# Kernel optimization log

Hardware: AMD Instinct MI355X
Metric: run time of the kernel (lower is better)

## Reference

```python
import jax, jax.numpy as jnp
import numpy as np

N = 4096
K = 8


def setup_inputs() -> dict:
    key = jax.random.key(0)
    kA, kb, ka, kZ, kC = jax.random.split(key, 5)
    A = (jax.random.uniform(kA, (N, N)) < 0.01).astype(jnp.float32)
    beta = jax.random.normal(kb, (N,), dtype=jnp.float32)
    a = jax.random.normal(ka, (1,), dtype=jnp.float32)
    Z = jax.random.normal(kZ, (K, N), dtype=jnp.float32)
    C = jax.random.normal(kC, (N, K), dtype=jnp.float32)
    return {"A": A, "beta": beta, "a": a, "Z": Z, "C": C}


def reference(A, beta, a, Z, C):
    # beta_ij = beta_i + beta_j  -> [N, N]
    beta2 = beta[:, None] + beta[None, :]
    Zs = jax.nn.softmax(Z, axis=0)          # [K, N], softmax over archetypes
    Cs = jax.nn.softmax(C, axis=0)          # [N, K], softmax over nodes
    # M = (Zs @ Cs @ Zs).T -> [N, K] latent positions
    M = (Zs @ (Cs @ Zs)).T
    # Pairwise euclidean distance with the original's +1e-6 shift inside the square.
    diff = M[:, None, :] - M[None, :, :] + 1e-6   # [N, N, K]
    z_dist = jnp.sqrt(jnp.sum(diff * diff, axis=-1))  # [N, N]
    theta = beta2 - a[0] * z_dist
    sp = jax.nn.softplus(theta)
    # Zero the diagonal (theta - diag(diagonal(theta)) zeroes diag entries).
    d = jnp.arange(N)
    theta_off = theta.at[d, d].set(0.0)
    sp_off = sp.at[d, d].set(0.0)
    LL = jnp.sum(theta_off * A) - jnp.sum(sp_off)
    return LL
```

## Files before the change

kernel.cpp:

```cpp
#include <hip/hip_runtime.h>

#define N 4096
#define K 8
#define RB 64
#define CB 256
#define RCH 16
#define NCH (RB / RCH)
#define NPB 16

__device__ __forceinline__ float fast_exp2(float x) { return __builtin_amdgcn_exp2f(x); }
__device__ __forceinline__ float fast_log2(float x) { return __builtin_amdgcn_logf(x); }
__device__ __forceinline__ float fast_sqrt(float x) { return __builtin_amdgcn_sqrtf(x); }

__device__ __forceinline__ void load_lds_16B(const float* g, float* l) {
    __builtin_amdgcn_global_load_lds((const __attribute__((address_space(1))) void*)g,
                                     (__attribute__((address_space(3))) void*)l,
                                     16, 0, 0);
}

__global__ __launch_bounds__(256) void prep_stats(
    const float* __restrict__ Z, const float* __restrict__ C,
    float* __restrict__ ZsT, float* __restrict__ Upart, float* __restrict__ out)
{
    const int t = threadIdx.x;
    const int n = blockIdx.x * 256 + t;
    const float L2E = 1.44269504f;

    __shared__ float zsL[256 * K];
    __shared__ float eL[256 * K];
    __shared__ float red[4][64];

    if (blockIdx.x == 0 && t == 0) out[0] = 0.f;

    float z[K];
#pragma unroll
    for (int k = 0; k < K; ++k) z[k] = Z[k * N + n];
    float zmax = z[0];
#pragma unroll
    for (int k = 1; k < K; ++k) zmax = fmaxf(zmax, z[k]);
    float zs[K];
    float zsum = 0.f;
#pragma unroll
    for (int k = 0; k < K; ++k) { zs[k] = fast_exp2((z[k] - zmax) * L2E); zsum += zs[k]; }
    const float inv = 1.f / zsum;
#pragma unroll
    for (int k = 0; k < K; ++k) zs[k] *= inv;

    float4* zst_p = (float4*)(ZsT + (size_t)n * K);
    zst_p[0] = make_float4(zs[0], zs[1], zs[2], zs[3]);
    zst_p[1] = make_float4(zs[4], zs[5], zs[6], zs[7]);

    const float4* c_p = (const float4*)(C + (size_t)n * K);
    const float4 c0 = c_p[0], c1 = c_p[1];
    float e[K];
    e[0] = fast_exp2(c0.x * L2E); e[1] = fast_exp2(c0.y * L2E);
    e[2] = fast_exp2(c0.z * L2E); e[3] = fast_exp2(c0.w * L2E);
    e[4] = fast_exp2(c1.x * L2E); e[5] = fast_exp2(c1.y * L2E);
    e[6] = fast_exp2(c1.z * L2E); e[7] = fast_exp2(c1.w * L2E);

#pragma unroll
    for (int k = 0; k < K; ++k) { zsL[t * K + k] = zs[k]; eL[t * K + k] = e[k]; }
    __syncthreads();

    const int cell = t & 63, q = t >> 6;
    const int a = cell >> 3, b = cell & 7;
    float s = 0.f;
    const int n0 = q * 64;
#pragma unroll 4
    for (int nn = 0; nn < 64; ++nn)
        s = fmaf(zsL[(n0 + nn) * K + a], eL[(n0 + nn) * K + b], s);
    red[q][cell] = s;
    __syncthreads();
    if (t < 64)
        Upart[blockIdx.x * 64 + t] = red[0][t] + red[1][t] + red[2][t] + red[3][t];
}

__global__ __launch_bounds__(256) void prep_M(
    const float* __restrict__ ZsT, const float* __restrict__ Upart,
    const float* __restrict__ A, const float* __restrict__ beta,
    const float* __restrict__ a_ptr, float* __restrict__ M,
    float* __restrict__ RowConst, float* __restrict__ out)
{
    const int t = threadIdx.x;
    const int n = blockIdx.x * 256 + t;
    const float L2E = 1.44269504f;
    const float LN2 = 0.69314718f;

    __shared__ float UL[64];
    __shared__ float SinvL[8];
    if (t < 64) {
        float s = 0.f;
#pragma unroll
        for (int blk = 0; blk < NPB; ++blk) s += Upart[blk * 64 + t];
        UL[t] = s;
    }
    __syncthreads();
    if (t < 8) {
        float s = 0.f;
#pragma unroll
        for (int a = 0; a < 8; ++a) s += UL[a * 8 + t];
        SinvL[t] = 1.f / s;
    }
    __syncthreads();

    const float4* zst_p = (const float4*)(ZsT + (size_t)n * K);
    const float4 z0 = zst_p[0], z1 = zst_p[1];
    float w[K];
    w[0] = z0.x * SinvL[0]; w[1] = z0.y * SinvL[1]; w[2] = z0.z * SinvL[2]; w[3] = z0.w * SinvL[3];
    w[4] = z1.x * SinvL[4]; w[5] = z1.y * SinvL[5]; w[6] = z1.z * SinvL[6]; w[7] = z1.w * SinvL[7];
    float m[K];
#pragma unroll
    for (int k = 0; k < K; ++k) {
        float acc = 0.f;
#pragma unroll
        for (int kk = 0; kk < K; ++kk) acc = fmaf(UL[k * K + kk], w[kk], acc);
        m[k] = acc;
    }
    float4* m_p = (float4*)(M + (size_t)n * K);
    m_p[0] = make_float4(m[0], m[1], m[2], m[3]);
    m_p[1] = make_float4(m[4], m[5], m[6], m[7]);

    float v[K];
    float s2 = 0.f;
#pragma unroll
    for (int k = 0; k < K; ++k) { v[k] = m[k] + 1e-6f; s2 = fmaf(v[k], v[k], s2); }
    float4* rc_p = (float4*)(RowConst + (size_t)n * 16);
    rc_p[0] = make_float4(-2.f * v[0], -2.f * v[1], -2.f * v[2], -2.f * v[3]);
    rc_p[1] = make_float4(-2.f * v[4], -2.f * v[5], -2.f * v[6], -2.f * v[7]);
    rc_p[2] = make_float4(s2, beta[n] * L2E, 0.f, 0.f);

    const float av = A[(size_t)n * N + n];
    const float theta = fmaf(-a_ptr[0], 2.8284271247e-6f, 2.f * beta[n]);
    const float ex = fast_exp2(theta * L2E);
    const float sp = LN2 * fast_log2(1.f + ex);
    float d = fmaf(theta, av, -sp);

    for (int off = 32; off > 0; off >>= 1) d += __shfl_down(d, off, 64);
    __shared__ float wsum[4];
    const int lane = t & 63, wid = t >> 6;
    if (lane == 0) wsum[wid] = d;
    __syncthreads();
    if (t == 0) atomicAdd(out, -(wsum[0] + wsum[1] + wsum[2] + wsum[3]));
}

__global__ __launch_bounds__(256) void pair_ll(
    const float* __restrict__ A, const float* __restrict__ beta,
    const float* __restrict__ a_ptr, const float* __restrict__ M,
    const float* __restrict__ RowConst, float* __restrict__ out)
{
    const int t = threadIdx.x;
    const int lane = t & 63, w = t >> 6;
    const int i0 = blockIdx.x * RB;
    const int jbase = blockIdx.y * CB;
    const int j = jbase + t;
    const float L2E = 1.44269504f;
    const float LN2 = 0.69314718f;

    __shared__ __align__(16) float Abuf[2][RCH][CB];
    __shared__ float wsum[4];

    const float4* mp = (const float4*)(M + (size_t)j * K);
    const float4 mj0 = mp[0], mj1 = mp[1];
    float mj2 = mj0.x * mj0.x;
    mj2 = fmaf(mj0.y, mj0.y, mj2); mj2 = fmaf(mj0.z, mj0.z, mj2);
    mj2 = fmaf(mj0.w, mj0.w, mj2); mj2 = fmaf(mj1.x, mj1.x, mj2);
    mj2 = fmaf(mj1.y, mj1.y, mj2); mj2 = fmaf(mj1.z, mj1.z, mj2);
    mj2 = fmaf(mj1.w, mj1.w, mj2);
    const float bjL2E = beta[j] * L2E;
    const float naL2E = -a_ptr[0] * L2E;

    {
        const float* g = A + (size_t)(i0 + w * 4) * N + jbase + lane * 4;
#pragma unroll
        for (int rr = 0; rr < 4; ++rr)
            load_lds_16B(g + (size_t)rr * N, &Abuf[0][w * 4 + rr][0]);
    }

    float acc_t = 0.f, acc_l = 0.f;
    int buf = 0;
    for (int c = 0; c < NCH; ++c) {
        __syncthreads();
        if (c + 1 < NCH) {
            const float* g = A + (size_t)(i0 + (c + 1) * RCH + w * 4) * N + jbase + lane * 4;
#pragma unroll
            for (int rr = 0; rr < 4; ++rr)
                load_lds_16B(g + (size_t)rr * N, &Abuf[buf ^ 1][w * 4 + rr][0]);
        }
#pragma unroll
        for (int r = 0; r < RCH; ++r) {
            const int ir = c * RCH + r;
            const float* rp = RowConst + (size_t)(i0 + ir) * 16;
            const float4 tm0 = *(const float4*)(rp);
            const float4 tm1 = *(const float4*)(rp + 4);
            const float2 cc  = *(const float2*)(rp + 8);
            const float av = Abuf[buf][r][t];
            float ss = cc.x + mj2;
            ss = fmaf(tm0.x, mj0.x, ss); ss = fmaf(tm0.y, mj0.y, ss);
            ss = fmaf(tm0.z, mj0.z, ss); ss = fmaf(tm0.w, mj0.w, ss);
            ss = fmaf(tm1.x, mj1.x, ss); ss = fmaf(tm1.y, mj1.y, ss);
            ss = fmaf(tm1.z, mj1.z, ss); ss = fmaf(tm1.w, mj1.w, ss);
            ss = fmaxf(ss, 0.f);
            const float dist = fast_sqrt(ss);
            const float t2 = fmaf(naL2E, dist, cc.y + bjL2E);
            const float ex = fast_exp2(t2);
            const float lp = fast_log2(1.f + ex);
            acc_t = fmaf(t2, av, acc_t);
            acc_l += lp;
        }
        buf ^= 1;
    }
    float acc = LN2 * (acc_t - acc_l);

    for (int off = 32; off > 0; off >>= 1) acc += __shfl_down(acc, off, 64);
    if (lane == 0) wsum[w] = acc;
    __syncthreads();
    if (t == 0) atomicAdd(out, wsum[0] + wsum[1] + wsum[2] + wsum[3]);
}

extern "C" void kernel_launch(void* const* d_in, const int* in_sizes, int n_in,
                              void* d_out, int out_size, void* d_ws, size_t ws_size,
                              hipStream_t stream)
{
    const float* A    = (const float*)d_in[0];
    const float* beta = (const float*)d_in[1];
    const float* a    = (const float*)d_in[2];
    const float* Z    = (const float*)d_in[3];
    const float* C    = (const float*)d_in[4];
    float* out = (float*)d_out;

    float* ws       = (float*)d_ws;
    float* ZsT      = ws;
    float* M        = ws + (size_t)N * K;
    float* Upart    = ws + (size_t)2 * N * K;
    float* RowConst = ws + (size_t)2 * N * K + NPB * 64;

    prep_stats<<<NPB, 256, 0, stream>>>(Z, C, ZsT, Upart, out);
    prep_M<<<NPB, 256, 0, stream>>>(ZsT, Upart, A, beta, a, M, RowConst, out);

    dim3 grid(N / RB, N / CB);
    pair_ll<<<grid, 256, 0, stream>>>(A, beta, a, M, RowConst, out);
}
```

Measured before the change: 115.1 us.

## Retile pair kernel to 16x1024 blocks with four columns per thread

Changes the pairwise tile from 64 rows x 256 columns to 16 rows x 1024 columns, with each thread handling four adjacent columns. Per-row constants are staged in LDS and reused across the four columns, and A is read from LDS as float4. The RowConst stride shrinks from 16 to 12 floats, and a launch-bounds occupancy hint is added. The aim is to amortise per-row constant loads and widen memory accesses, at the cost of more registers per thread for the four column vectors.

```diff
diff --git a/kernel.cpp b/kernel.cpp
--- a/kernel.cpp
+++ b/kernel.cpp
@@ -2,9 +2,9 @@
 
 #define N 4096
 #define K 8
-#define RB 64
-#define CB 256
-#define RCH 16
+#define RB 16
+#define CB 1024
+#define RCH 4
 #define NCH (RB / RCH)
 #define NPB 16
 
@@ -124,7 +124,7 @@
     float s2 = 0.f;
 #pragma unroll
     for (int k = 0; k < K; ++k) { v[k] = m[k] + 1e-6f; s2 = fmaf(v[k], v[k], s2); }
-    float4* rc_p = (float4*)(RowConst + (size_t)n * 16);
+    float4* rc_p = (float4*)(RowConst + (size_t)n * 12);
     rc_p[0] = make_float4(-2.f * v[0], -2.f * v[1], -2.f * v[2], -2.f * v[3]);
     rc_p[1] = make_float4(-2.f * v[4], -2.f * v[5], -2.f * v[6], -2.f * v[7]);
     rc_p[2] = make_float4(s2, beta[n] * L2E, 0.f, 0.f);
@@ -143,7 +143,7 @@
     if (t == 0) atomicAdd(out, -(wsum[0] + wsum[1] + wsum[2] + wsum[3]));
 }
 
-__global__ __launch_bounds__(256) void pair_ll(
+__global__ __launch_bounds__(256, 4) void pair_ll(
     const float* __restrict__ A, const float* __restrict__ beta,
     const float* __restrict__ a_ptr, const float* __restrict__ M,
     const float* __restrict__ RowConst, float* __restrict__ out)
@@ -152,28 +152,42 @@
     const int lane = t & 63, w = t >> 6;
     const int i0 = blockIdx.x * RB;
     const int jbase = blockIdx.y * CB;
-    const int j = jbase + t;
+    const int j0 = jbase + 4 * t;
     const float L2E = 1.44269504f;
     const float LN2 = 0.69314718f;
 
     __shared__ __align__(16) float Abuf[2][RCH][CB];
+    __shared__ __align__(16) float cL[RB][12];
     __shared__ float wsum[4];
 
-    const float4* mp = (const float4*)(M + (size_t)j * K);
-    const float4 mj0 = mp[0], mj1 = mp[1];
-    float mj2 = mj0.x * mj0.x;
-    mj2 = fmaf(mj0.y, mj0.y, mj2); mj2 = fmaf(mj0.z, mj0.z, mj2);
-    mj2 = fmaf(mj0.w, mj0.w, mj2); mj2 = fmaf(mj1.x, mj1.x, mj2);
-    mj2 = fmaf(mj1.y, mj1.y, mj2); mj2 = fmaf(mj1.z, mj1.z, mj2);
-    mj2 = fmaf(mj1.w, mj1.w, mj2);
-    const float bjL2E = beta[j] * L2E;
+    if (t < RB) {
+        const float4* rp = (const float4*)(RowConst + (size_t)(i0 + t) * 12);
+        float4* dp = (float4*)&cL[t][0];
+        dp[0] = rp[0]; dp[1] = rp[1]; dp[2] = rp[2];
+    }
+
+    float4 mj0[4], mj1[4];
+    float mj2[4];
+#pragma unroll
+    for (int c = 0; c < 4; ++c) {
+        const float4* mp = (const float4*)(M + (size_t)(j0 + c) * K);
+        mj0[c] = mp[0]; mj1[c] = mp[1];
+        float s2 = mj0[c].x * mj0[c].x;
+        s2 = fmaf(mj0[c].y, mj0[c].y, s2); s2 = fmaf(mj0[c].z, mj0[c].z, s2);
+        s2 = fmaf(mj0[c].w, mj0[c].w, s2); s2 = fmaf(mj1[c].x, mj1[c].x, s2);
+        s2 = fmaf(mj1[c].y, mj1[c].y, s2); s2 = fmaf(mj1[c].z, mj1[c].z, s2);
+        s2 = fmaf(mj1[c].w, mj1[c].w, s2);
+        mj2[c] = s2;
+    }
+    const float4 bj4 = *(const float4*)(beta + j0);
+    float bj2[4] = { bj4.x * L2E, bj4.y * L2E, bj4.z * L2E, bj4.w * L2E };
     const float naL2E = -a_ptr[0] * L2E;
 
     {
-        const float* g = A + (size_t)(i0 + w * 4) * N + jbase + lane * 4;
-#pragma unroll
-        for (int rr = 0; rr < 4; ++rr)
-            load_lds_16B(g + (size_t)rr * N, &Abuf[0][w * 4 + rr][0]);
+        const float* g = A + (size_t)(i0 + w) * N + jbase + lane * 4;
+#pragma unroll
+        for (int s = 0; s < 4; ++s)
+            load_lds_16B(g + s * 256, &Abuf[0][w][s * 256]);
     }
 
     float acc_t = 0.f, acc_l = 0.f;
@@ -181,31 +195,34 @@
     for (int c = 0; c < NCH; ++c) {
         __syncthreads();
         if (c + 1 < NCH) {
-            const float* g = A + (size_t)(i0 + (c + 1) * RCH + w * 4) * N + jbase + lane * 4;
-#pragma unroll
-            for (int rr = 0; rr < 4; ++rr)
-                load_lds_16B(g + (size_t)rr * N, &Abuf[buf ^ 1][w * 4 + rr][0]);
+            const float* g = A + (size_t)(i0 + (c + 1) * RCH + w) * N + jbase + lane * 4;
+#pragma unroll
+            for (int s = 0; s < 4; ++s)
+                load_lds_16B(g + s * 256, &Abuf[buf ^ 1][w][s * 256]);
         }
 #pragma unroll
         for (int r = 0; r < RCH; ++r) {
             const int ir = c * RCH + r;
-            const float* rp = RowConst + (size_t)(i0 + ir) * 16;
-            const float4 tm0 = *(const float4*)(rp);
-            const float4 tm1 = *(const float4*)(rp + 4);
-            const float2 cc  = *(const float2*)(rp + 8);
-            const float av = Abuf[buf][r][t];
-            float ss = cc.x + mj2;
-            ss = fmaf(tm0.x, mj0.x, ss); ss = fmaf(tm0.y, mj0.y, ss);
-            ss = fmaf(tm0.z, mj0.z, ss); ss = fmaf(tm0.w, mj0.w, ss);
-            ss = fmaf(tm1.x, mj1.x, ss); ss = fmaf(tm1.y, mj1.y, ss);
-            ss = fmaf(tm1.z, mj1.z, ss); ss = fmaf(tm1.w, mj1.w, ss);
-            ss = fmaxf(ss, 0.f);
-            const float dist = fast_sqrt(ss);
-            const float t2 = fmaf(naL2E, dist, cc.y + bjL2E);
-            const float ex = fast_exp2(t2);
-            const float lp = fast_log2(1.f + ex);
-            acc_t = fmaf(t2, av, acc_t);
-            acc_l += lp;
+            const float4 av  = *(const float4*)(&Abuf[buf][r][4 * t]);
+            const float4 tm0 = *(const float4*)(&cL[ir][0]);
+            const float4 tm1 = *(const float4*)(&cL[ir][4]);
+            const float4 ccv = *(const float4*)(&cL[ir][8]);
+            const float avc[4] = { av.x, av.y, av.z, av.w };
+#pragma unroll
+            for (int cc2 = 0; cc2 < 4; ++cc2) {
+                float ss = ccv.x + mj2[cc2];
+                ss = fmaf(tm0.x, mj0[cc2].x, ss); ss = fmaf(tm0.y, mj0[cc2].y, ss);
+                ss = fmaf(tm0.z, mj0[cc2].z, ss); ss = fmaf(tm0.w, mj0[cc2].w, ss);
+                ss = fmaf(tm1.x, mj1[cc2].x, ss); ss = fmaf(tm1.y, mj1[cc2].y, ss);
+                ss = fmaf(tm1.z, mj1[cc2].z, ss); ss = fmaf(tm1.w, mj1[cc2].w, ss);
+                ss = fmaxf(ss, 0.f);
+                const float dist = fast_sqrt(ss);
+                const float t2 = fmaf(naL2E, dist, ccv.y + bj2[cc2]);
+                const float ex = fast_exp2(t2);
+                const float lp = fast_log2(1.f + ex);
+                acc_t = fmaf(t2, avc[cc2], acc_t);
+                acc_l += lp;
+            }
         }
         buf ^= 1;
     }
```

Measured after the change: 114.4 us. Within noise of the previous version (-0.6%).
